# Performance work log

Hardware: AMD Instinct MI355X
Metric: run time of the kernel (lower is better)

The kernel has to match this reference:

```python
import jax, jax.numpy as jnp
import numpy as np

MAX_DELAY = 48          # delay buffer depth
D1 = MAX_DELAY + 1
SIGMA = MAX_DELAY / 2.0
MAX_THINK = 8           # config.max_think_steps
NUM_CLASSES = 63
VOCAB = NUM_CLASSES + 1 # vocab includes think-end token
THINK_END = NUM_CLASSES
H = 512                 # hidden_size
B = 8                   # batch
T = 48                  # encoder time steps


def _calc_credit(tau):
    # relu(-|(d - clip(tau,1,D)) * (1/sigma)^2| + 1/sigma), shape (D1,H,H)
    tc = jnp.clip(tau, 1.0, float(MAX_DELAY))[None]
    d = jnp.arange(D1, dtype=tau.dtype)[:, None, None]
    inv = 1.0 / SIGMA
    return jax.nn.relu(inv - jnp.abs((d - tc) * (inv * inv)))


def _forward(x, wa, ba, lat, tau, we, be, N):
    cm = _calc_credit(tau) * lat[None]   # (D1,H,H), constant across steps
    d_idx = jnp.arange(D1)

    def step_b(buf, ptr, x_t):           # buf (D1,Bx,H), x_t (Bx,VOCAB)
        h_del = jax.lax.dynamic_index_in_dim(buf, ptr, 0, keepdims=False)
        h = jnp.tanh(x_t @ wa.T + ba + h_del)
        scat = jnp.einsum('dhi,bi->dbh', cm, h)
        shifted = scat[(d_idx - ptr) % D1]                      # roll by +ptr along d
        buf = (buf + shifted) * (d_idx != ptr).astype(buf.dtype)[:, None, None]
        y = h_del @ we.T + be
        return buf, (ptr + 1) % D1, y

    def step_1(buf, ptr, x_t):           # per-sample: buf (D1,H), x_t (VOCAB,)
        h_del = jax.lax.dynamic_index_in_dim(buf, ptr, 0, keepdims=False)
        h = jnp.tanh(wa @ x_t + ba + h_del)
        scat = jnp.einsum('dhi,i->dh', cm, h)
        shifted = scat[(d_idx - ptr) % D1]
        buf = (buf + shifted) * (d_idx != ptr).astype(buf.dtype)[:, None]
        y = we @ h_del + be
        return buf, (ptr + 1) % D1, y

    def gumbel_hard(y, k):               # F.gumbel_softmax(tau=1, hard=True)
        u = jax.random.uniform(k, y.shape, minval=1e-9, maxval=1.0)
        logits = y - jnp.log(-jnp.log(u))
        soft = jax.nn.softmax(logits)
        idx = jnp.argmax(logits)
        hard = jax.nn.one_hot(idx, VOCAB, dtype=y.dtype)
        return hard + soft - jax.lax.stop_gradient(soft), idx

    bsz = x.shape[0]
    buf0 = jnp.zeros((D1, bsz, H), x.dtype)

    def enc(carry, x_t):
        buf, ptr = carry
        buf, ptr, _ = step_b(buf, ptr, x_t)
        return (buf, ptr), None

    (buf, ptr), _ = jax.lax.scan(enc, (buf0, jnp.int32(0)), jnp.swapaxes(x, 0, 1))

    def decode_one(buf_i, x_last, key_i):
        # bounded think loop (original while-loop, max MAX_THINK+1 iterations)
        def think(carry, i):
            b, cur, p, done = carry
            nb, np_, y = step_1(b, p, cur)
            ncur, idx = gumbel_hard(y, jax.random.fold_in(key_i, i))
            b = jnp.where(done, b, nb)
            cur = jnp.where(done, cur, ncur)
            p = jnp.where(done, p, np_)
            done = done | (idx == THINK_END) | (i + 1 > MAX_THINK)
            return (b, cur, p, done), None
        (b, cur, p, _), _ = jax.lax.scan(
            think, (buf_i, x_last, ptr, jnp.bool_(False)), jnp.arange(MAX_THINK + 1))

        def dec(carry, j):
            b, cur, p = carry
            b, p, y = step_1(b, p, cur)
            ncur, _ = gumbel_hard(y, jax.random.fold_in(key_i, 10000 + j))
            return (b, ncur, p), y
        _, ys = jax.lax.scan(dec, (b, cur, p), jnp.arange(N))
        return ys                        # (N, VOCAB)

    keys = jax.random.split(jax.random.key(42), bsz)
    ys = jax.vmap(decode_one, in_axes=(1, 0, 0))(buf, x[:, -1, :], keys)
    return ys[:, :, :-1]                 # drop think-end logit


def setup_inputs() -> dict:
    key = jax.random.key(0)
    ks = jax.random.split(key, 6)
    x = jax.random.normal(ks[0], (B, T, VOCAB), dtype=jnp.float32)
    lim_a = (6.0 / (VOCAB + H)) ** 0.5
    w_afferent = jax.random.uniform(ks[1], (H, VOCAB), minval=-lim_a, maxval=lim_a)
    b_afferent = jnp.zeros((H,), jnp.float32)
    lim_l = (6.0 / (H + H)) ** 0.5
    lateral = jax.random.uniform(ks[2], (H, H), minval=-lim_l, maxval=lim_l)
    tau = MAX_DELAY * jax.random.uniform(ks[3], (H, H)) + 1.0
    lim_e = (6.0 / (H + VOCAB)) ** 0.5
    w_efferent = jax.random.uniform(ks[4], (VOCAB, H), minval=-lim_e, maxval=lim_e)
    b_efferent = jnp.zeros((VOCAB,), jnp.float32)
    return {"x": x, "w_afferent": w_afferent, "b_afferent": b_afferent,
            "lateral": lateral, "tau": tau,
            "w_efferent": w_efferent, "b_efferent": b_efferent, "N": T - 3}


def reference(x, w_afferent, b_afferent, lateral, tau, w_efferent, b_efferent, N):
    return _forward(x, w_afferent, b_afferent, lateral, tau, w_efferent, b_efferent, N)
```

## Files before the change

### kernel.cpp

```cpp
#include <hip/hip_runtime.h>
#include <stdint.h>

namespace {

constexpr int H = 512, V = 64, B = 8, T = 48, D1 = 49, NDEC = 45, NSTEP = 102;
constexpr int NBLK = 256, TPB = 512;
constexpr int NG = 8, GMEM = NBLK / NG;

constexpr size_t OFF_PUB  = 0;
constexpr size_t OFF_IDX  = 131072;
constexpr size_t OFF_PFLG = 132096;
constexpr size_t OFF_YPF  = 132352;
constexpr size_t OFF_YF   = 132416;
constexpr size_t OFF_BAR  = 132544;
constexpr size_t OFF_YP   = 133056;
constexpr size_t OFF_XW   = 149440;

__device__ __forceinline__ float ldA(const float* p) {
  return __hip_atomic_load(p, __ATOMIC_RELAXED, __HIP_MEMORY_SCOPE_AGENT);
}
__device__ __forceinline__ void stA(float* p, float v) {
  __hip_atomic_store(p, v, __ATOMIC_RELAXED, __HIP_MEMORY_SCOPE_AGENT);
}
__device__ __forceinline__ int ldAi(const int* p) {
  return __hip_atomic_load(p, __ATOMIC_RELAXED, __HIP_MEMORY_SCOPE_AGENT);
}
__device__ __forceinline__ void stAi(int* p, int v) {
  __hip_atomic_store(p, v, __ATOMIC_RELAXED, __HIP_MEMORY_SCOPE_AGENT);
}

__device__ __forceinline__ void tf2x32(uint32_t k0, uint32_t k1,
                                       uint32_t& x0, uint32_t& x1) {
  const uint32_t ks2 = k0 ^ k1 ^ 0x1BD11BDAu;
  x0 += k0; x1 += k1;
#define RR(r) { x0 += x1; x1 = (x1 << (r)) | (x1 >> (32-(r))); x1 ^= x0; }
  RR(13) RR(15) RR(26) RR(6)  x0 += k1;  x1 += ks2 + 1u;
  RR(17) RR(29) RR(16) RR(24) x0 += ks2; x1 += k0 + 2u;
  RR(13) RR(15) RR(26) RR(6)  x0 += k0;  x1 += k1 + 3u;
  RR(17) RR(29) RR(16) RR(24) x0 += k1;  x1 += ks2 + 4u;
  RR(13) RR(15) RR(26) RR(6)  x0 += ks2; x1 += k0 + 5u;
#undef RR
}

__device__ __forceinline__ float gumbel_from_bits(uint32_t bits) {
  float u = __uint_as_float((bits >> 9) | 0x3F800000u) - 1.0f;
  u = u + 1e-9f;
  return -logf(-logf(u));
}

__global__ __launch_bounds__(512) void k_zero(float* __restrict__ ws) {
  int* ib = (int*)ws;
  for (size_t i = OFF_PFLG + threadIdx.x; i < OFF_BAR + 512; i += 512)
    stAi(&ib[i], 0);
  for (int i = threadIdx.x; i < 32768; i += 512) stA(&ws[i], 0.0f);
}

__device__ __forceinline__ void gbar(int* bar, int grp, int ep) {
  asm volatile("s_waitcnt vmcnt(0)" ::: "memory");
  __syncthreads();
  if (threadIdx.x == 0) {
    int old = __hip_atomic_fetch_add(&bar[16 + 16 * grp], 1,
                                     __ATOMIC_RELAXED, __HIP_MEMORY_SCOPE_AGENT);
    if (((old + 1) & (GMEM - 1)) == 0) {
      int oldG = __hip_atomic_fetch_add(&bar[0], 1,
                                        __ATOMIC_RELAXED, __HIP_MEMORY_SCOPE_AGENT);
      if (((oldG + 1) & (NG - 1)) == 0) {
        #pragma unroll
        for (int q = 0; q < NG; ++q) stAi(&bar[160 + 16 * q], ep);
      }
    }
    int guard = 0;
    while (ldAi(&bar[160 + 16 * grp]) < ep) {
      __builtin_amdgcn_s_sleep(2);
      if (++guard > (1 << 20)) break;
    }
  }
  __syncthreads();
}

__global__ __launch_bounds__(TPB, 4)
void k_main(
    const float* __restrict__ x,  const float* __restrict__ wa,
    const float* __restrict__ ba, const float* __restrict__ lat,
    const float* __restrict__ tau,const float* __restrict__ we,
    const float* __restrict__ be, float* __restrict__ ws,
    float* __restrict__ out) {
  const int blk = blockIdx.x, tid = threadIdx.x;
  float* pub = ws + OFF_PUB;
  float* yp  = ws + OFF_YP;
  float* xw  = ws + OFF_XW;
  int* idxA  = (int*)ws + OFF_IDX;
  int* pflag = (int*)ws + OFF_PFLG;
  int* ypf   = (int*)ws + OFF_YPF;
  int* yf    = (int*)ws + OFF_YF;
  int* bar   = (int*)ws + OFF_BAR;

  const int p  = blk >> 5;
  const int g  = blk & 31;
  const int w  = tid >> 6, lane = tid & 63;
  const int cb = p * 64;
  const bool isG0  = (g == 0);
  const bool isFin = (g == 31);
  const int fb = p;

  __shared__ float s_h[8 * 64];
  __shared__ float s_hd2[8 * 64];
  __shared__ float s_tc[16 * 64];
  __shared__ float s_lat[16 * 64];
  __shared__ float s_buf[8 * 16 * 49];
  __shared__ float s_snap[128];
  __shared__ int   s_ptr[8], s_cidx[8], s_done8[8];

  for (int q2 = tid; q2 < 8 * 16 * 49; q2 += TPB) s_buf[q2] = 0.0f;
  for (int q2 = tid; q2 < 16 * 64; q2 += TPB) {
    int hl = q2 >> 6, ii = q2 & 63;
    int ho = g * 16 + hl, i = cb + ii;
    float tv = tau[(size_t)ho * H + i];
    s_tc[q2]  = fminf(fmaxf(tv, 1.0f), 48.0f);
    s_lat[q2] = lat[(size_t)ho * H + i];
  }
  if (tid < 8) { s_ptr[tid] = 0; s_cidx[tid] = 0; s_done8[tid] = 0; }
  if (g < 24) {
    #pragma unroll
    for (int tt = 0; tt < 2; ++tt) {
      int t0 = g * 2 + tt;
      int b = (tid >> 6) & 7, il = tid & 63;
      int j = cb + il;
      const float* xr = x + ((size_t)b * T + t0) * V;
      const float* war = wa + (size_t)j * V;
      float acc = 0.0f;
      #pragma unroll
      for (int v = 0; v < V; v += 4) {
        float4 w4 = *(const float4*)(war + v);
        float4 x4 = *(const float4*)(xr + v);
        acc = fmaf(w4.x, x4.x, acc); acc = fmaf(w4.y, x4.y, acc);
        acc = fmaf(w4.z, x4.z, acc); acc = fmaf(w4.w, x4.w, acc);
      }
      stA(&xw[((size_t)t0 * 8 + b) * 512 + j], acc);
    }
  }
  uint32_t ka = 0u, kb = (uint32_t)fb;
  tf2x32(0u, 42u, ka, kb);

  gbar(bar, blk % NG, 1);

  for (int t = 0; t < NSTEP; ++t) {
    const bool thinkM = (t >= T && t < T + 9);
    const bool decM   = (t >= T + 9);
    const int needY   = (t - 1 >= T) ? 1 : 0;

    if (tid < 64) {
      int guard = 0;
      while (true) {
        int pred = 1;
        if (lane < 32)      pred = (ldAi(&pflag[p * 32 + lane]) >= t);
        else if (lane < 40 && needY) pred = (ldAi(&yf[lane - 32]) >= t - 1);
        if (__all(pred)) break;
        __builtin_amdgcn_s_sleep(1);
        if (++guard > (1 << 22)) break;
      }
    }
    __syncthreads();
    asm volatile("" ::: "memory");

    if (tid < 8 && t >= 1) {
      const int b = tid;
      const bool prevThink = (t - 1 >= T) && (t - 1 < T + 9);
      const bool aP = prevThink ? (s_done8[b] == 0) : true;
      if (t - 1 >= T) {
        int ix = ldAi(&idxA[(t - 1) * 8 + b]);
        if (aP) s_cidx[b] = ix;
        if (prevThink && (ix == 63 || (t - 1 - T) == 8)) s_done8[b] = 1;
      }
      if (aP) { int pv = s_ptr[b]; s_ptr[b] = (pv + 1 == D1) ? 0 : pv + 1; }
    }
    __syncthreads();

    int actM = 0;
    #pragma unroll
    for (int b = 0; b < B; ++b)
      actM |= ((thinkM ? (s_done8[b] ^ 1) : 1) & 1) << b;

    {
      int il = tid & 63, b = tid >> 6;
      int j = cb + il;
      const float* pr = pub + ((size_t)(t & 3) * 32768 + (size_t)j * 64 + b * 8);
      float p0 = ldA(pr),     p1 = ldA(pr + 1), p2 = ldA(pr + 2), p3 = ldA(pr + 3);
      float p4 = ldA(pr + 4), p5 = ldA(pr + 5), p6 = ldA(pr + 6), p7 = ldA(pr + 7);
      float hd = ((p0 + p1) + (p2 + p3)) + ((p4 + p5) + (p6 + p7));
      if (isG0 && t >= T) s_hd2[b * 64 + il] = hd;
      float acc;
      if (t <= T) {
        int xrow = (t < T) ? t : (T - 1);
        acc = (ba[j] + hd) + ldA(&xw[((size_t)xrow * 8 + b) * 512 + j]);
      } else {
        acc = (ba[j] + hd) + wa[(size_t)j * V + s_cidx[b]];
      }
      s_h[b * 64 + il] = tanhf(acc);
    }
    if (tid < 128) {
      int hl = tid >> 3, b = tid & 7;
      int sn = ((actM >> b) & 1) ? s_ptr[b] + 1 : s_ptr[b];
      if (sn >= D1) sn -= D1;
      s_snap[tid] = s_buf[(b * 16 + hl) * 49 + sn];
    }
    __syncthreads();

    if (w == 0) {
      const float dd = 1.0f;
      const float inv = 1.0f / 24.0f, inv2 = inv * inv;
      #pragma unroll
      for (int half = 0; half < 2; ++half) {
        int m = lane + half * 64;
        int hl = m >> 3, b = m & 7;
        float val = s_snap[m];
        if ((actM >> b) & 1) {
          float acc = 0.0f;
          const float* tcr = &s_tc[hl * 64];
          const float* ltr = &s_lat[hl * 64];
          const float* hr  = &s_h[b * 64];
          #pragma unroll 4
          for (int ii = 0; ii < 64; ii += 4) {
            float4 t4 = *(const float4*)(tcr + ii);
            float4 l4 = *(const float4*)(ltr + ii);
            float4 h4 = *(const float4*)(hr + ii);
            float q0 = fmaxf(0.0f, inv - fabsf((dd - t4.x) * inv2)) * l4.x;
            acc = fmaf(q0, h4.x, acc);
            float q1 = fmaxf(0.0f, inv - fabsf((dd - t4.y) * inv2)) * l4.y;
            acc = fmaf(q1, h4.y, acc);
            float q2 = fmaxf(0.0f, inv - fabsf((dd - t4.z) * inv2)) * l4.z;
            acc = fmaf(q2, h4.z, acc);
            float q3 = fmaxf(0.0f, inv - fabsf((dd - t4.w) * inv2)) * l4.w;
            acc = fmaf(q3, h4.w, acc);
          }
          val = val + acc;
        }
        stA(&pub[(size_t)((t + 1) & 3) * 32768
                 + (size_t)(g * 16 + hl) * 64 + b * 8 + p], val);
      }
      asm volatile("s_waitcnt vmcnt(0)" ::: "memory");
      if (lane == 0) stAi(&pflag[g * 8 + p], t + 1);
    }

    if (w == 1) {
      if (isG0 && t >= T) {
        int o = lane;
        const float* wer = we + (size_t)o * H + cb;
        #pragma unroll
        for (int b = 0; b < 8; ++b) {
          const float* hp = &s_hd2[b * 64];
          float a2 = 0.0f;
          #pragma unroll 4
          for (int i2 = 0; i2 < 64; i2 += 4) {
            float4 w4 = *(const float4*)(wer + i2);
            a2 = fmaf(w4.x, hp[i2],     a2); a2 = fmaf(w4.y, hp[i2 + 1], a2);
            a2 = fmaf(w4.z, hp[i2 + 2], a2); a2 = fmaf(w4.w, hp[i2 + 3], a2);
          }
          stA(&yp[(size_t)(t & 3) * 4096 + (size_t)p * 512 + b * 64 + o], a2);
        }
        asm volatile("s_waitcnt vmcnt(0)" ::: "memory");
        if (lane == 0) stAi(&ypf[p], t);
      }
      if (isFin && t >= T) {
        const int o = lane, it = t - T;
        if (o < 8) {
          int guard = 0;
          while (ldAi(&ypf[o]) < t) {
            __builtin_amdgcn_s_sleep(1);
            if (++guard > (1 << 22)) break;
          }
        }
        asm volatile("" ::: "memory");
        const float* ypr = yp + (size_t)(t & 3) * 4096 + fb * 64 + o;
        float y0 = ldA(ypr),        y1 = ldA(ypr + 512);
        float y2 = ldA(ypr + 1024), y3 = ldA(ypr + 1536);
        float y4 = ldA(ypr + 2048), y5 = ldA(ypr + 2560);
        float y6 = ldA(ypr + 3072), y7 = ldA(ypr + 3584);
        float y = (((y0 + y1) + (y2 + y3)) + ((y4 + y5) + (y6 + y7))) + be[o];
        if (decM && o < V - 1)
          out[((size_t)fb * NDEC + (t - T - 9)) * (V - 1) + o] = y;
        uint32_t data = (it < 9) ? (uint32_t)it : (uint32_t)(10000 + (it - 9));
        uint32_t e = 0u, f = data; tf2x32(ka, kb, e, f);
        uint32_t r0 = 0u, r1 = (uint32_t)o; tf2x32(e, f, r0, r1);
        float bv = y + gumbel_from_bits(r0 ^ r1);
        int bi = o;
        #pragma unroll
        for (int m2 = 32; m2 >= 1; m2 >>= 1) {
          float ov = __shfl_xor(bv, m2, 64);
          int   oi = __shfl_xor(bi, m2, 64);
          if (ov > bv || (ov == bv && oi < bi)) { bv = ov; bi = oi; }
        }
        if (o == 0) {
          stAi(&idxA[t * 8 + fb], bi);
          asm volatile("s_waitcnt vmcnt(0)" ::: "memory");
          stAi(&yf[fb], t);
        }
      }
    }

    {
      const float dd = (float)lane;
      const float inv = 1.0f / 24.0f, inv2 = inv * inv;
      float accA[8], accB[8];
      #pragma unroll
      for (int b = 0; b < B; ++b) { accA[b] = 0.0f; accB[b] = 0.0f; }
      const float* tcA = &s_tc[(w * 2) * 64];
      const float* ltA = &s_lat[(w * 2) * 64];
      const float* tcB = &s_tc[(w * 2 + 1) * 64];
      const float* ltB = &s_lat[(w * 2 + 1) * 64];
      #pragma unroll 4
      for (int ii = 0; ii < 64; ii += 4) {
        float4 tA = *(const float4*)(tcA + ii);
        float4 lA = *(const float4*)(ltA + ii);
        float4 tB = *(const float4*)(tcB + ii);
        float4 lB = *(const float4*)(ltB + ii);
        float qA[4], qB[4];
        #pragma unroll
        for (int k = 0; k < 4; ++k) {
          float ta = ((const float*)&tA)[k];
          qA[k] = fmaxf(0.0f, inv - fabsf((dd - ta) * inv2)) * ((const float*)&lA)[k];
          float tb = ((const float*)&tB)[k];
          qB[k] = fmaxf(0.0f, inv - fabsf((dd - tb) * inv2)) * ((const float*)&lB)[k];
        }
        #pragma unroll
        for (int b = 0; b < B; ++b) {
          float4 h4 = *(const float4*)(&s_h[b * 64 + ii]);
          const float* hp = (const float*)&h4;
          #pragma unroll
          for (int k = 0; k < 4; ++k) accA[b] = fmaf(qA[k], hp[k], accA[b]);
          #pragma unroll
          for (int k = 0; k < 4; ++k) accB[b] = fmaf(qB[k], hp[k], accB[b]);
        }
      }
      if (lane >= 1 && lane <= 48) {
        #pragma unroll
        for (int b = 0; b < B; ++b) {
          if ((actM >> b) & 1) {
            int slot = s_ptr[b] + lane; if (slot >= D1) slot -= D1;
            int aA = (b * 16 + w * 2) * 49 + slot;
            float oA = s_buf[aA];
            s_buf[aA] = (lane == 48) ? accA[b] : (oA + accA[b]);
            int aB = (b * 16 + w * 2 + 1) * 49 + slot;
            float oB = s_buf[aB];
            s_buf[aB] = (lane == 48) ? accB[b] : (oB + accB[b]);
          }
        }
      }
    }
    __syncthreads();
  }
}

}

extern "C" void kernel_launch(void* const* d_in, const int* in_sizes, int n_in,
                              void* d_out, int out_size, void* d_ws, size_t ws_size,
                              hipStream_t stream) {
  (void)in_sizes; (void)n_in; (void)out_size; (void)ws_size;
  const float* x   = (const float*)d_in[0];
  const float* wa  = (const float*)d_in[1];
  const float* ba  = (const float*)d_in[2];
  const float* lat = (const float*)d_in[3];
  const float* tau = (const float*)d_in[4];
  const float* we  = (const float*)d_in[5];
  const float* be  = (const float*)d_in[6];
  float* out = (float*)d_out;
  float* ws  = (float*)d_ws;

  k_zero<<<dim3(1), dim3(512), 0, stream>>>(ws);
  k_main<<<dim3(NBLK), dim3(TPB), 0, stream>>>(x, wa, ba, lat, tau, we, be, ws, out);
}
```

Before: 1.608 ms.

## Warp-specialize step loop: 4 wavefronts do scatter, others handle publish/output

The per-step work is redistributed so wavefronts 0-3 each compute four rows of the delay-buffer scatter (instead of all eight doing two rows each), while wavefronts 4, 5 and 6 handle the critical publish, the efferent partial products and the final gumbel/argmax respectively. The publish path no longer waits behind the scatter computation in the same wavefront, shortening the cross-block dependency chain. Shared arrays are padded to a row stride of 68 to reduce LDS bank conflicts. The cost is fewer wavefronts on the bulk scatter FMAs, with higher register pressure from the 32 accumulators per lane.

New measurement: 1.676 ms. 1.04x slower.

```diff
diff --git a/kernel.cpp b/kernel.cpp
--- a/kernel.cpp
+++ b/kernel.cpp
@@ -6,6 +6,7 @@
 constexpr int H = 512, V = 64, B = 8, T = 48, D1 = 49, NDEC = 45, NSTEP = 102;
 constexpr int NBLK = 256, TPB = 512;
 constexpr int NG = 8, GMEM = NBLK / NG;
+constexpr int LW = 68;
 
 constexpr size_t OFF_PUB  = 0;
 constexpr size_t OFF_IDX  = 131072;
@@ -103,10 +104,10 @@
   const bool isFin = (g == 31);
   const int fb = p;
 
-  __shared__ float s_h[8 * 64];
+  __shared__ float s_h[8 * LW];
   __shared__ float s_hd2[8 * 64];
-  __shared__ float s_tc[16 * 64];
-  __shared__ float s_lat[16 * 64];
+  __shared__ float s_tc[16 * LW];
+  __shared__ float s_lat[16 * LW];
   __shared__ float s_buf[8 * 16 * 49];
   __shared__ float s_snap[128];
   __shared__ int   s_ptr[8], s_cidx[8], s_done8[8];
@@ -116,8 +117,8 @@
     int hl = q2 >> 6, ii = q2 & 63;
     int ho = g * 16 + hl, i = cb + ii;
     float tv = tau[(size_t)ho * H + i];
-    s_tc[q2]  = fminf(fmaxf(tv, 1.0f), 48.0f);
-    s_lat[q2] = lat[(size_t)ho * H + i];
+    s_tc[hl * LW + ii]  = fminf(fmaxf(tv, 1.0f), 48.0f);
+    s_lat[hl * LW + ii] = lat[(size_t)ho * H + i];
   }
   if (tid < 8) { s_ptr[tid] = 0; s_cidx[tid] = 0; s_done8[tid] = 0; }
   if (g < 24) {
@@ -196,7 +197,7 @@
       } else {
         acc = (ba[j] + hd) + wa[(size_t)j * V + s_cidx[b]];
       }
-      s_h[b * 64 + il] = tanhf(acc);
+      s_h[b * LW + il] = tanhf(acc);
     }
     if (tid < 128) {
       int hl = tid >> 3, b = tid & 7;
@@ -206,7 +207,55 @@
     }
     __syncthreads();
 
-    if (w == 0) {
+    if (w < 4) {
+      const float dd = (float)lane;
+      const float inv = 1.0f / 24.0f, inv2 = inv * inv;
+      float acc[4][8];
+      #pragma unroll
+      for (int r = 0; r < 4; ++r)
+        #pragma unroll
+        for (int b = 0; b < 8; ++b) acc[r][b] = 0.0f;
+      const float* tc0 = &s_tc[(w * 4) * LW];
+      const float* lt0 = &s_lat[(w * 4) * LW];
+      #pragma unroll 2
+      for (int ii = 0; ii < 64; ii += 4) {
+        float q[4][4];
+        #pragma unroll
+        for (int r = 0; r < 4; ++r) {
+          float4 t4 = *(const float4*)(tc0 + r * LW + ii);
+          float4 l4 = *(const float4*)(lt0 + r * LW + ii);
+          q[r][0] = fmaxf(0.0f, inv - fabsf((dd - t4.x) * inv2)) * l4.x;
+          q[r][1] = fmaxf(0.0f, inv - fabsf((dd - t4.y) * inv2)) * l4.y;
+          q[r][2] = fmaxf(0.0f, inv - fabsf((dd - t4.z) * inv2)) * l4.z;
+          q[r][3] = fmaxf(0.0f, inv - fabsf((dd - t4.w) * inv2)) * l4.w;
+        }
+        #pragma unroll
+        for (int b = 0; b < 8; ++b) {
+          float4 h4 = *(const float4*)(&s_h[b * LW + ii]);
+          const float* hp = (const float*)&h4;
+          #pragma unroll
+          for (int r = 0; r < 4; ++r) {
+            #pragma unroll
+            for (int k = 0; k < 4; ++k)
+              acc[r][b] = fmaf(q[r][k], hp[k], acc[r][b]);
+          }
+        }
+      }
+      if (lane >= 1 && lane <= 48) {
+        #pragma unroll
+        for (int b = 0; b < 8; ++b) {
+          if ((actM >> b) & 1) {
+            int slot = s_ptr[b] + lane; if (slot >= D1) slot -= D1;
+            #pragma unroll
+            for (int r = 0; r < 4; ++r) {
+              int a = (b * 16 + w * 4 + r) * 49 + slot;
+              float o2 = s_buf[a];
+              s_buf[a] = (lane == 48) ? acc[r][b] : (o2 + acc[r][b]);
+            }
+          }
+        }
+      }
+    } else if (w == 4) {
       const float dd = 1.0f;
       const float inv = 1.0f / 24.0f, inv2 = inv * inv;
       #pragma unroll
@@ -216,9 +265,9 @@
         float val = s_snap[m];
         if ((actM >> b) & 1) {
           float acc = 0.0f;
-          const float* tcr = &s_tc[hl * 64];
-          const float* ltr = &s_lat[hl * 64];
-          const float* hr  = &s_h[b * 64];
+          const float* tcr = &s_tc[hl * LW];
+          const float* ltr = &s_lat[hl * LW];
+          const float* hr  = &s_h[b * LW];
           #pragma unroll 4
           for (int ii = 0; ii < 64; ii += 4) {
             float4 t4 = *(const float4*)(tcr + ii);
@@ -240,9 +289,7 @@
       }
       asm volatile("s_waitcnt vmcnt(0)" ::: "memory");
       if (lane == 0) stAi(&pflag[g * 8 + p], t + 1);
-    }
-
-    if (w == 1) {
+    } else if (w == 5) {
       if (isG0 && t >= T) {
         int o = lane;
         const float* wer = we + (size_t)o * H + cb;
@@ -261,6 +308,7 @@
         asm volatile("s_waitcnt vmcnt(0)" ::: "memory");
         if (lane == 0) stAi(&ypf[p], t);
       }
+    } else if (w == 6) {
       if (isFin && t >= T) {
         const int o = lane, it = t - T;
         if (o < 8) {
@@ -298,55 +346,6 @@
       }
     }
 
-    {
-      const float dd = (float)lane;
-      const float inv = 1.0f / 24.0f, inv2 = inv * inv;
-      float accA[8], accB[8];
-      #pragma unroll
-      for (int b = 0; b < B; ++b) { accA[b] = 0.0f; accB[b] = 0.0f; }
-      const float* tcA = &s_tc[(w * 2) * 64];
-      const float* ltA = &s_lat[(w * 2) * 64];
-      const float* tcB = &s_tc[(w * 2 + 1) * 64];
-      const float* ltB = &s_lat[(w * 2 + 1) * 64];
-      #pragma unroll 4
-      for (int ii = 0; ii < 64; ii += 4) {
-        float4 tA = *(const float4*)(tcA + ii);
-        float4 lA = *(const float4*)(ltA + ii);
-        float4 tB = *(const float4*)(tcB + ii);
-        float4 lB = *(const float4*)(ltB + ii);
-        float qA[4], qB[4];
-        #pragma unroll
-        for (int k = 0; k < 4; ++k) {
-          float ta = ((const float*)&tA)[k];
-          qA[k] = fmaxf(0.0f, inv - fabsf((dd - ta) * inv2)) * ((const float*)&lA)[k];
-          float tb = ((const float*)&tB)[k];
-          qB[k] = fmaxf(0.0f, inv - fabsf((dd - tb) * inv2)) * ((const float*)&lB)[k];
-        }
-        #pragma unroll
-        for (int b = 0; b < B; ++b) {
-          float4 h4 = *(const float4*)(&s_h[b * 64 + ii]);
-          const float* hp = (const float*)&h4;
-          #pragma unroll
-          for (int k = 0; k < 4; ++k) accA[b] = fmaf(qA[k], hp[k], accA[b]);
-          #pragma unroll
-          for (int k = 0; k < 4; ++k) accB[b] = fmaf(qB[k], hp[k], accB[b]);
-        }
-      }
-      if (lane >= 1 && lane <= 48) {
-        #pragma unroll
-        for (int b = 0; b < B; ++b) {
-          if ((actM >> b) & 1) {
-            int slot = s_ptr[b] + lane; if (slot >= D1) slot -= D1;
-            int aA = (b * 16 + w * 2) * 49 + slot;
-            float oA = s_buf[aA];
-            s_buf[aA] = (lane == 48) ? accA[b] : (oA + accA[b]);
-            int aB = (b * 16 + w * 2 + 1) * 49 + slot;
-            float oB = s_buf[aB];
-            s_buf[aB] = (lane == 48) ? accB[b] : (oB + accB[b]);
-          }
-        }
-      }
-    }
     __syncthreads();
   }
 }
```
